# Optimization experiments

Measured on AMD Instinct MI355X. Metric: run time of the kernel, lower is better.

Reference implementation:

```python
import jax, jax.numpy as jnp
import numpy as np

N_STREAMS = 8192
ITERS = 5
EPS = 1e-6


def setup_inputs() -> dict:
    key = jax.random.key(0)
    # matches torch init: randn(n, n) * 0.1
    logits = jax.random.normal(key, (N_STREAMS, N_STREAMS), dtype=jnp.float32) * 0.1
    return {"logits": logits}


def reference(logits) -> jnp.ndarray:
    n = logits.shape[0]
    # M = sigmoid(logits) + I
    M = jax.nn.sigmoid(logits) + jnp.eye(n, dtype=logits.dtype)
    for _ in range(ITERS):
        M = M / (jnp.sum(M, axis=1, keepdims=True) + EPS)  # row normalize
        M = M / (jnp.sum(M, axis=0, keepdims=True) + EPS)  # col normalize
    return M
```

## Files before the change

### kernel.cpp

```cpp
#include <hip/hip_runtime.h>

#define N_DIM 8192
#define EPS 1e-6f

__device__ __forceinline__ float bflo(unsigned u) { return __uint_as_float(u << 16); }
__device__ __forceinline__ float bfhi(unsigned u) { return __uint_as_float(u & 0xffff0000u); }
__device__ __forceinline__ unsigned f2bf_bits(float f) {
    unsigned u = __float_as_uint(f);
    return (u + 0x7fffu + ((u >> 16) & 1u)) >> 16;
}
__device__ __forceinline__ float sigmoidf_fast(float x) {
    return 1.f / (1.f + __expf(-x));
}

__device__ __forceinline__ float block_reduce_256(float acc) {
    #pragma unroll
    for (int off = 32; off > 0; off >>= 1) acc += __shfl_down(acc, off, 64);
    __shared__ float sred[4];
    const int lane = threadIdx.x & 63;
    const int wid  = threadIdx.x >> 6;
    if (lane == 0) sred[wid] = acc;
    __syncthreads();
    return sred[0] + sred[1] + sred[2] + sred[3];
}

__global__ __launch_bounds__(256) void k_init(const float* __restrict__ logits,
                                              unsigned short* __restrict__ B,
                                              float* __restrict__ r,
                                              float* __restrict__ cvec) {
    const int row = blockIdx.x;
    const float4* lrow = (const float4*)(logits + (size_t)row * N_DIM);
    uint4* brow = (uint4*)(B + (size_t)row * N_DIM);
    float acc = 0.f;
    #pragma unroll
    for (int it = 0; it < 4; ++it) {
        const int v = it * 256 + (int)threadIdx.x;
        const float4 x0 = lrow[2 * v];
        const float4 x1 = lrow[2 * v + 1];
        float s[8] = { sigmoidf_fast(x0.x), sigmoidf_fast(x0.y),
                       sigmoidf_fast(x0.z), sigmoidf_fast(x0.w),
                       sigmoidf_fast(x1.x), sigmoidf_fast(x1.y),
                       sigmoidf_fast(x1.z), sigmoidf_fast(x1.w) };
        const int j = v * 8;
        #pragma unroll
        for (int k = 0; k < 8; ++k)
            if (j + k == row) s[k] += 1.f;
        unsigned b[8];
        #pragma unroll
        for (int k = 0; k < 8; ++k) {
            b[k] = f2bf_bits(s[k]);
            acc += __uint_as_float(b[k] << 16);
        }
        brow[v] = make_uint4(b[0] | (b[1] << 16), b[2] | (b[3] << 16),
                             b[4] | (b[5] << 16), b[6] | (b[7] << 16));
    }
    const float t = block_reduce_256(acc);
    if (threadIdx.x == 0) {
        r[row]   = 1.f / (t + EPS);
        cvec[row] = 1.f;
    }
}

__global__ __launch_bounds__(256) void k_row(const unsigned short* __restrict__ B,
                                             const float* __restrict__ cvec,
                                             float* __restrict__ r) {
    const int row = blockIdx.x;
    const uint4* brow = (const uint4*)(B + (size_t)row * N_DIM);
    const float4* cv = (const float4*)cvec;
    float acc = 0.f;
    #pragma unroll
    for (int it = 0; it < 4; ++it) {
        const int v = it * 256 + (int)threadIdx.x;
        const uint4 b = brow[v];
        const float4 c0 = cv[2 * v];
        const float4 c1 = cv[2 * v + 1];
        acc += bflo(b.x) * c0.x + bfhi(b.x) * c0.y
             + bflo(b.y) * c0.z + bfhi(b.y) * c0.w
             + bflo(b.z) * c1.x + bfhi(b.z) * c1.y
             + bflo(b.w) * c1.z + bfhi(b.w) * c1.w;
    }
    const float t = block_reduce_256(acc);
    if (threadIdx.x == 0) {
        const float rv = r[row];
        r[row] = rv / (rv * t + EPS);
    }
}

__global__ __launch_bounds__(256) void k_col(const unsigned short* __restrict__ B,
                                             const float* __restrict__ r,
                                             float* __restrict__ partial) {
    const int cb = blockIdx.x & 3;
    const int rb = blockIdx.x >> 2;
    const int col0 = cb * 2048 + (int)threadIdx.x * 8;
    float a[8] = {0.f, 0.f, 0.f, 0.f, 0.f, 0.f, 0.f, 0.f};
    const int i0 = rb * 64;
    for (int i = i0; i < i0 + 64; ++i) {
        const uint4 b = *(const uint4*)(B + (size_t)i * N_DIM + col0);
        const float ri = r[i];
        a[0] += bflo(b.x) * ri; a[1] += bfhi(b.x) * ri;
        a[2] += bflo(b.y) * ri; a[3] += bfhi(b.y) * ri;
        a[4] += bflo(b.z) * ri; a[5] += bfhi(b.z) * ri;
        a[6] += bflo(b.w) * ri; a[7] += bfhi(b.w) * ri;
    }
    float* p = partial + (size_t)rb * N_DIM + col0;
    ((float4*)p)[0] = make_float4(a[0], a[1], a[2], a[3]);
    ((float4*)p)[1] = make_float4(a[4], a[5], a[6], a[7]);
}

__global__ __launch_bounds__(256) void k_cupd(const float* __restrict__ partial,
                                              float* __restrict__ cvec) {
    __shared__ float s[4][64];
    const int tc = threadIdx.x & 63;
    const int tg = threadIdx.x >> 6;
    const int j = blockIdx.x * 64 + tc;
    float u = 0.f;
    #pragma unroll 4
    for (int rb = tg * 32; rb < tg * 32 + 32; ++rb)
        u += partial[(size_t)rb * N_DIM + j];
    s[tg][tc] = u;
    __syncthreads();
    if (threadIdx.x < 64) {
        const float tot = s[0][tc] + s[1][tc] + s[2][tc] + s[3][tc];
        const float cj = cvec[j];
        cvec[j] = cj / (cj * tot + EPS);
    }
}

__global__ __launch_bounds__(256) void k_out(const float* __restrict__ logits,
                                             const float* __restrict__ r,
                                             const float* __restrict__ cvec,
                                             float* __restrict__ out) {
    const int row = blockIdx.x;
    const float ri = r[row];
    const float4* lrow = (const float4*)(logits + (size_t)row * N_DIM);
    const float4* cv = (const float4*)cvec;
    float4* orow = (float4*)(out + (size_t)row * N_DIM);
    #pragma unroll
    for (int it = 0; it < 8; ++it) {
        const int v = it * 256 + (int)threadIdx.x;
        const float4 x = lrow[v];
        const float4 cc = cv[v];
        const int j = v * 4;
        float s0 = sigmoidf_fast(x.x); if (j     == row) s0 += 1.f;
        float s1 = sigmoidf_fast(x.y); if (j + 1 == row) s1 += 1.f;
        float s2 = sigmoidf_fast(x.z); if (j + 2 == row) s2 += 1.f;
        float s3 = sigmoidf_fast(x.w); if (j + 3 == row) s3 += 1.f;
        orow[v] = make_float4(s0 * ri * cc.x, s1 * ri * cc.y,
                              s2 * ri * cc.z, s3 * ri * cc.w);
    }
}

extern "C" void kernel_launch(void* const* d_in, const int* in_sizes, int n_in,
                              void* d_out, int out_size, void* d_ws, size_t ws_size,
                              hipStream_t stream) {
    const float* logits = (const float*)d_in[0];
    float* out = (float*)d_out;
    unsigned short* B = (unsigned short*)(out + (size_t)N_DIM * N_DIM / 2);
    float* r      = (float*)d_ws;
    float* cvec   = r + N_DIM;
    float* partial = cvec + N_DIM;

    const dim3 blk(256);
    k_init<<<dim3(N_DIM), blk, 0, stream>>>(logits, B, r, cvec);
    for (int it = 0; it < 5; ++it) {
        if (it > 0) k_row<<<dim3(N_DIM), blk, 0, stream>>>(B, cvec, r);
        k_col<<<dim3(512), blk, 0, stream>>>(B, r, partial);
        k_cupd<<<dim3(128), blk, 0, stream>>>(partial, cvec);
    }
    k_out<<<dim3(N_DIM), blk, 0, stream>>>(logits, r, cvec, out);
}
```

Baseline: 759.0 us.

## Fuse row and column normalization passes over row strips, reuse bf16 matrix in output

Each block now processes a strip of 16 rows. It computes the row sums, updates r, and accumulates the r-weighted column partials from the same registers, so every iteration reads the bf16 matrix once instead of twice. The init kernel is fused with the first column pass in the same way. When the workspace is large enough, the output kernel rebuilds values from the bf16 copy instead of recomputing sigmoid from the fp32 logits. The cost is more partial rows (512 instead of 128) that the column update must reduce, and an output built from bf16 values, which lowers precision.

```diff
diff --git a/kernel.cpp b/kernel.cpp
--- a/kernel.cpp
+++ b/kernel.cpp
@@ -2,6 +2,8 @@
 
 #define N_DIM 8192
 #define EPS 1e-6f
+#define R_STRIP 16
+#define NRB (N_DIM / R_STRIP)
 
 __device__ __forceinline__ float bflo(unsigned u) { return __uint_as_float(u << 16); }
 __device__ __forceinline__ float bfhi(unsigned u) { return __uint_as_float(u & 0xffff0000u); }
@@ -12,124 +14,190 @@
 __device__ __forceinline__ float sigmoidf_fast(float x) {
     return 1.f / (1.f + __expf(-x));
 }
-
-__device__ __forceinline__ float block_reduce_256(float acc) {
-    #pragma unroll
-    for (int off = 32; off > 0; off >>= 1) acc += __shfl_down(acc, off, 64);
-    __shared__ float sred[4];
-    const int lane = threadIdx.x & 63;
-    const int wid  = threadIdx.x >> 6;
-    if (lane == 0) sred[wid] = acc;
-    __syncthreads();
-    return sred[0] + sred[1] + sred[2] + sred[3];
+__device__ __forceinline__ float dot8(uint4 b, float4 c0, float4 c1) {
+    return bflo(b.x) * c0.x + bfhi(b.x) * c0.y + bflo(b.y) * c0.z + bfhi(b.y) * c0.w
+         + bflo(b.z) * c1.x + bfhi(b.z) * c1.y + bflo(b.w) * c1.z + bfhi(b.w) * c1.w;
+}
+__device__ __forceinline__ void acc8(float* a, uint4 b, float rr) {
+    a[0] += bflo(b.x) * rr; a[1] += bfhi(b.x) * rr;
+    a[2] += bflo(b.y) * rr; a[3] += bfhi(b.y) * rr;
+    a[4] += bflo(b.z) * rr; a[5] += bfhi(b.z) * rr;
+    a[6] += bflo(b.w) * rr; a[7] += bfhi(b.w) * rr;
+}
+__device__ __forceinline__ uint4 sig_pack8(float4 x0, float4 x1, int jbase, int row, float& t) {
+    float s[8] = { sigmoidf_fast(x0.x), sigmoidf_fast(x0.y), sigmoidf_fast(x0.z), sigmoidf_fast(x0.w),
+                   sigmoidf_fast(x1.x), sigmoidf_fast(x1.y), sigmoidf_fast(x1.z), sigmoidf_fast(x1.w) };
+    #pragma unroll
+    for (int k = 0; k < 8; ++k)
+        if (jbase + k == row) s[k] += 1.f;
+    unsigned b[8];
+    #pragma unroll
+    for (int k = 0; k < 8; ++k) {
+        b[k] = f2bf_bits(s[k]);
+        t += __uint_as_float(b[k] << 16);
+    }
+    return make_uint4(b[0] | (b[1] << 16), b[2] | (b[3] << 16),
+                      b[4] | (b[5] << 16), b[6] | (b[7] << 16));
 }
 
 __global__ __launch_bounds__(256) void k_init(const float* __restrict__ logits,
                                               unsigned short* __restrict__ B,
                                               float* __restrict__ r,
-                                              float* __restrict__ cvec) {
+                                              float* __restrict__ partial) {
+    __shared__ float sred[2][4];
+    const int tid = threadIdx.x;
+    const int lane = tid & 63, wid = tid >> 6;
+    const int i0 = blockIdx.x * R_STRIP;
+    float a[4][8];
+    #pragma unroll
+    for (int s = 0; s < 4; ++s)
+        #pragma unroll
+        for (int k = 0; k < 8; ++k) a[s][k] = 0.f;
+
+    for (int bb = 0; bb < R_STRIP / 2; ++bb) {
+        const int row0 = i0 + 2 * bb, row1 = row0 + 1;
+        const float4* l0 = (const float4*)(logits + (size_t)row0 * N_DIM);
+        const float4* l1 = (const float4*)(logits + (size_t)row1 * N_DIM);
+        uint4* w0 = (uint4*)(B + (size_t)row0 * N_DIM);
+        uint4* w1 = (uint4*)(B + (size_t)row1 * N_DIM);
+        uint4 b0[4], b1[4];
+        float t0 = 0.f, t1 = 0.f;
+        #pragma unroll
+        for (int s = 0; s < 4; ++s) {
+            const int v = s * 256 + tid;
+            b0[s] = sig_pack8(l0[2 * v], l0[2 * v + 1], v * 8, row0, t0);
+            b1[s] = sig_pack8(l1[2 * v], l1[2 * v + 1], v * 8, row1, t1);
+            w0[v] = b0[s];
+            w1[v] = b1[s];
+        }
+        #pragma unroll
+        for (int off = 32; off > 0; off >>= 1) {
+            t0 += __shfl_down(t0, off, 64);
+            t1 += __shfl_down(t1, off, 64);
+        }
+        if (lane == 0) { sred[0][wid] = t0; sred[1][wid] = t1; }
+        __syncthreads();
+        const float T0 = sred[0][0] + sred[0][1] + sred[0][2] + sred[0][3];
+        const float T1 = sred[1][0] + sred[1][1] + sred[1][2] + sred[1][3];
+        const float r0 = 1.f / (T0 + EPS);
+        const float r1 = 1.f / (T1 + EPS);
+        __syncthreads();
+        if (tid == 0) { r[row0] = r0; r[row1] = r1; }
+        #pragma unroll
+        for (int s = 0; s < 4; ++s) { acc8(a[s], b0[s], r0); acc8(a[s], b1[s], r1); }
+    }
+    float* p = partial + (size_t)blockIdx.x * N_DIM;
+    #pragma unroll
+    for (int s = 0; s < 4; ++s) {
+        const int col = s * 2048 + tid * 8;
+        *(float4*)(p + col)     = make_float4(a[s][0], a[s][1], a[s][2], a[s][3]);
+        *(float4*)(p + col + 4) = make_float4(a[s][4], a[s][5], a[s][6], a[s][7]);
+    }
+}
+
+__global__ __launch_bounds__(256) void k_fused(const unsigned short* __restrict__ B,
+                                               const float* __restrict__ cvec,
+                                               float* __restrict__ r,
+                                               float* __restrict__ partial) {
+    __shared__ float sred[2][4];
+    const int tid = threadIdx.x;
+    const int lane = tid & 63, wid = tid >> 6;
+    const int i0 = blockIdx.x * R_STRIP;
+    const float4* cv = (const float4*)cvec;
+    float a[4][8];
+    #pragma unroll
+    for (int s = 0; s < 4; ++s)
+        #pragma unroll
+        for (int k = 0; k < 8; ++k) a[s][k] = 0.f;
+
+    for (int bb = 0; bb < R_STRIP / 2; ++bb) {
+        const int row0 = i0 + 2 * bb, row1 = row0 + 1;
+        const float r0old = r[row0];
+        const float r1old = r[row1];
+        const uint4* br0 = (const uint4*)(B + (size_t)row0 * N_DIM);
+        const uint4* br1 = (const uint4*)(B + (size_t)row1 * N_DIM);
+        uint4 b0[4], b1[4];
+        float t0 = 0.f, t1 = 0.f;
+        #pragma unroll
+        for (int s = 0; s < 4; ++s) {
+            const int v = s * 256 + tid;
+            b0[s] = br0[v];
+            b1[s] = br1[v];
+            const float4 c0 = cv[2 * v];
+            const float4 c1 = cv[2 * v + 1];
+            t0 += dot8(b0[s], c0, c1);
+            t1 += dot8(b1[s], c0, c1);
+        }
+        #pragma unroll
+        for (int off = 32; off > 0; off >>= 1) {
+            t0 += __shfl_down(t0, off, 64);
+            t1 += __shfl_down(t1, off, 64);
+        }
+        if (lane == 0) { sred[0][wid] = t0; sred[1][wid] = t1; }
+        __syncthreads();
+        const float T0 = sred[0][0] + sred[0][1] + sred[0][2] + sred[0][3];
+        const float T1 = sred[1][0] + sred[1][1] + sred[1][2] + sred[1][3];
+        const float r0 = r0old / (r0old * T0 + EPS);
+        const float r1 = r1old / (r1old * T1 + EPS);
+        __syncthreads();
+        if (tid == 0) { r[row0] = r0; r[row1] = r1; }
+        #pragma unroll
+        for (int s = 0; s < 4; ++s) { acc8(a[s], b0[s], r0); acc8(a[s], b1[s], r1); }
+    }
+    float* p = partial + (size_t)blockIdx.x * N_DIM;
+    #pragma unroll
+    for (int s = 0; s < 4; ++s) {
+        const int col = s * 2048 + tid * 8;
+        *(float4*)(p + col)     = make_float4(a[s][0], a[s][1], a[s][2], a[s][3]);
+        *(float4*)(p + col + 4) = make_float4(a[s][4], a[s][5], a[s][6], a[s][7]);
+    }
+}
+
+__global__ __launch_bounds__(256) void k_cupd(const float* __restrict__ partial,
+                                              float* __restrict__ cvec, int first) {
+    __shared__ float s[4][64];
+    const int tc = threadIdx.x & 63;
+    const int tg = threadIdx.x >> 6;
+    const int j = blockIdx.x * 64 + tc;
+    float u = 0.f;
+    #pragma unroll 8
+    for (int rb = tg * (NRB / 4); rb < (tg + 1) * (NRB / 4); ++rb)
+        u += partial[(size_t)rb * N_DIM + j];
+    s[tg][tc] = u;
+    __syncthreads();
+    if (threadIdx.x < 64) {
+        const float tot = s[0][tc] + s[1][tc] + s[2][tc] + s[3][tc];
+        const float cj = first ? 1.f : cvec[j];
+        cvec[j] = cj / (cj * tot + EPS);
+    }
+}
+
+__global__ __launch_bounds__(256) void k_out(const unsigned short* __restrict__ B,
+                                             const float* __restrict__ r,
+                                             const float* __restrict__ cvec,
+                                             float* __restrict__ out) {
     const int row = blockIdx.x;
-    const float4* lrow = (const float4*)(logits + (size_t)row * N_DIM);
-    uint4* brow = (uint4*)(B + (size_t)row * N_DIM);
-    float acc = 0.f;
-    #pragma unroll
-    for (int it = 0; it < 4; ++it) {
-        const int v = it * 256 + (int)threadIdx.x;
-        const float4 x0 = lrow[2 * v];
-        const float4 x1 = lrow[2 * v + 1];
-        float s[8] = { sigmoidf_fast(x0.x), sigmoidf_fast(x0.y),
-                       sigmoidf_fast(x0.z), sigmoidf_fast(x0.w),
-                       sigmoidf_fast(x1.x), sigmoidf_fast(x1.y),
-                       sigmoidf_fast(x1.z), sigmoidf_fast(x1.w) };
-        const int j = v * 8;
-        #pragma unroll
-        for (int k = 0; k < 8; ++k)
-            if (j + k == row) s[k] += 1.f;
-        unsigned b[8];
-        #pragma unroll
-        for (int k = 0; k < 8; ++k) {
-            b[k] = f2bf_bits(s[k]);
-            acc += __uint_as_float(b[k] << 16);
-        }
-        brow[v] = make_uint4(b[0] | (b[1] << 16), b[2] | (b[3] << 16),
-                             b[4] | (b[5] << 16), b[6] | (b[7] << 16));
-    }
-    const float t = block_reduce_256(acc);
-    if (threadIdx.x == 0) {
-        r[row]   = 1.f / (t + EPS);
-        cvec[row] = 1.f;
-    }
-}
-
-__global__ __launch_bounds__(256) void k_row(const unsigned short* __restrict__ B,
-                                             const float* __restrict__ cvec,
-                                             float* __restrict__ r) {
-    const int row = blockIdx.x;
+    const float ri = r[row];
     const uint4* brow = (const uint4*)(B + (size_t)row * N_DIM);
     const float4* cv = (const float4*)cvec;
-    float acc = 0.f;
+    float* orow = out + (size_t)row * N_DIM;
     #pragma unroll
     for (int it = 0; it < 4; ++it) {
         const int v = it * 256 + (int)threadIdx.x;
         const uint4 b = brow[v];
         const float4 c0 = cv[2 * v];
         const float4 c1 = cv[2 * v + 1];
-        acc += bflo(b.x) * c0.x + bfhi(b.x) * c0.y
-             + bflo(b.y) * c0.z + bfhi(b.y) * c0.w
-             + bflo(b.z) * c1.x + bfhi(b.z) * c1.y
-             + bflo(b.w) * c1.z + bfhi(b.w) * c1.w;
-    }
-    const float t = block_reduce_256(acc);
-    if (threadIdx.x == 0) {
-        const float rv = r[row];
-        r[row] = rv / (rv * t + EPS);
-    }
-}
-
-__global__ __launch_bounds__(256) void k_col(const unsigned short* __restrict__ B,
-                                             const float* __restrict__ r,
-                                             float* __restrict__ partial) {
-    const int cb = blockIdx.x & 3;
-    const int rb = blockIdx.x >> 2;
-    const int col0 = cb * 2048 + (int)threadIdx.x * 8;
-    float a[8] = {0.f, 0.f, 0.f, 0.f, 0.f, 0.f, 0.f, 0.f};
-    const int i0 = rb * 64;
-    for (int i = i0; i < i0 + 64; ++i) {
-        const uint4 b = *(const uint4*)(B + (size_t)i * N_DIM + col0);
-        const float ri = r[i];
-        a[0] += bflo(b.x) * ri; a[1] += bfhi(b.x) * ri;
-        a[2] += bflo(b.y) * ri; a[3] += bfhi(b.y) * ri;
-        a[4] += bflo(b.z) * ri; a[5] += bfhi(b.z) * ri;
-        a[6] += bflo(b.w) * ri; a[7] += bfhi(b.w) * ri;
-    }
-    float* p = partial + (size_t)rb * N_DIM + col0;
-    ((float4*)p)[0] = make_float4(a[0], a[1], a[2], a[3]);
-    ((float4*)p)[1] = make_float4(a[4], a[5], a[6], a[7]);
-}
-
-__global__ __launch_bounds__(256) void k_cupd(const float* __restrict__ partial,
-                                              float* __restrict__ cvec) {
-    __shared__ float s[4][64];
-    const int tc = threadIdx.x & 63;
-    const int tg = threadIdx.x >> 6;
-    const int j = blockIdx.x * 64 + tc;
-    float u = 0.f;
-    #pragma unroll 4
-    for (int rb = tg * 32; rb < tg * 32 + 32; ++rb)
-        u += partial[(size_t)rb * N_DIM + j];
-    s[tg][tc] = u;
-    __syncthreads();
-    if (threadIdx.x < 64) {
-        const float tot = s[0][tc] + s[1][tc] + s[2][tc] + s[3][tc];
-        const float cj = cvec[j];
-        cvec[j] = cj / (cj * tot + EPS);
-    }
-}
-
-__global__ __launch_bounds__(256) void k_out(const float* __restrict__ logits,
-                                             const float* __restrict__ r,
-                                             const float* __restrict__ cvec,
-                                             float* __restrict__ out) {
+        *(float4*)(orow + v * 8)     = make_float4(bflo(b.x) * ri * c0.x, bfhi(b.x) * ri * c0.y,
+                                                   bflo(b.y) * ri * c0.z, bfhi(b.y) * ri * c0.w);
+        *(float4*)(orow + v * 8 + 4) = make_float4(bflo(b.z) * ri * c1.x, bfhi(b.z) * ri * c1.y,
+                                                   bflo(b.w) * ri * c1.z, bfhi(b.w) * ri * c1.w);
+    }
+}
+
+__global__ __launch_bounds__(256) void k_out_logits(const float* __restrict__ logits,
+                                                    const float* __restrict__ r,
+                                                    const float* __restrict__ cvec,
+                                                    float* __restrict__ out) {
     const int row = blockIdx.x;
     const float ri = r[row];
     const float4* lrow = (const float4*)(logits + (size_t)row * N_DIM);
@@ -145,8 +213,7 @@
         float s1 = sigmoidf_fast(x.y); if (j + 1 == row) s1 += 1.f;
         float s2 = sigmoidf_fast(x.z); if (j + 2 == row) s2 += 1.f;
         float s3 = sigmoidf_fast(x.w); if (j + 3 == row) s3 += 1.f;
-        orow[v] = make_float4(s0 * ri * cc.x, s1 * ri * cc.y,
-                              s2 * ri * cc.z, s3 * ri * cc.w);
+        orow[v] = make_float4(s0 * ri * cc.x, s1 * ri * cc.y, s2 * ri * cc.z, s3 * ri * cc.w);
     }
 }
 
@@ -155,17 +222,31 @@
                               hipStream_t stream) {
     const float* logits = (const float*)d_in[0];
     float* out = (float*)d_out;
-    unsigned short* B = (unsigned short*)(out + (size_t)N_DIM * N_DIM / 2);
-    float* r      = (float*)d_ws;
-    float* cvec   = r + N_DIM;
-    float* partial = cvec + N_DIM;
+    const size_t nn = (size_t)N_DIM * N_DIM;
+    const size_t need = nn * 2 + (2 * N_DIM + (size_t)NRB * N_DIM) * 4;
+    const bool use_ws = ws_size >= need + 256;
+    float* wsf = (float*)d_ws;
+    unsigned short* B;
+    float *r, *cvec, *partial;
+    if (use_ws) {
+        B = (unsigned short*)wsf;
+        r = wsf + nn / 2;
+    } else {
+        B = (unsigned short*)(out + nn / 2);
+        r = wsf;
+    }
+    cvec = r + N_DIM;
+    partial = cvec + N_DIM;
 
     const dim3 blk(256);
-    k_init<<<dim3(N_DIM), blk, 0, stream>>>(logits, B, r, cvec);
-    for (int it = 0; it < 5; ++it) {
-        if (it > 0) k_row<<<dim3(N_DIM), blk, 0, stream>>>(B, cvec, r);
-        k_col<<<dim3(512), blk, 0, stream>>>(B, r, partial);
-        k_cupd<<<dim3(128), blk, 0, stream>>>(partial, cvec);
-    }
-    k_out<<<dim3(N_DIM), blk, 0, stream>>>(logits, r, cvec, out);
-}
+    k_init<<<dim3(NRB), blk, 0, stream>>>(logits, B, r, partial);
+    k_cupd<<<dim3(128), blk, 0, stream>>>(partial, cvec, 1);
+    for (int it = 1; it < 5; ++it) {
+        k_fused<<<dim3(NRB), blk, 0, stream>>>(B, cvec, r, partial);
+        k_cupd<<<dim3(128), blk, 0, stream>>>(partial, cvec, 0);
+    }
+    if (use_ws)
+        k_out<<<dim3(N_DIM), blk, 0, stream>>>(B, r, cvec, out);
+    else
+        k_out_logits<<<dim3(N_DIM), blk, 0, stream>>>(logits, r, cvec, out);
+}
```

After: 635.6 us. -16.3%, faster.
